# Kernel tuning notes

Measured on AMD Instinct MI355X. Metric: run time of the kernel, lower is better.

## Reference

```python
import math
import jax, jax.numpy as jnp
import numpy as np

EMBED_DIM = 512
NUM_HEADS = 8
HEAD_DIM = EMBED_DIM // NUM_HEADS
NUM_EDGE_TYPES = 10
N = 2048  # nodes
B = 1


def setup_inputs() -> dict:
    key = jax.random.key(0)
    ks = jax.random.split(key, 8)
    s = 1.0 / math.sqrt(EMBED_DIM)
    return {
        "query": jax.random.normal(ks[0], (N, B, EMBED_DIM), jnp.float32),
        "key": jax.random.normal(ks[1], (N, B, EMBED_DIM), jnp.float32),
        "value": jax.random.normal(ks[2], (N, B, EMBED_DIM), jnp.float32),
        "edge_id_mat": jax.random.randint(ks[3], (N, N), 0, NUM_EDGE_TYPES, jnp.int32),
        "in_proj_weight": jax.random.normal(ks[4], (3 * EMBED_DIM, EMBED_DIM), jnp.float32) * s,
        "in_proj_bias": jnp.zeros((3 * EMBED_DIM,), jnp.float32),
        "out_proj_weight": jax.random.normal(ks[5], (EMBED_DIM, EMBED_DIM), jnp.float32) * s,
        "out_proj_bias": jnp.zeros((EMBED_DIM,), jnp.float32),
        "edge_embs_K": jax.random.normal(ks[6], (NUM_EDGE_TYPES, HEAD_DIM), jnp.float32),
    }


def reference(query, key, value, edge_id_mat, in_proj_weight, in_proj_bias,
              out_proj_weight, out_proj_bias, edge_embs_K):
    L, Bsz, E = query.shape
    H, hd = NUM_HEADS, HEAD_DIM
    w_q, w_k, w_v = jnp.split(in_proj_weight, 3, axis=0)
    b_q, b_k, b_v = jnp.split(in_proj_bias, 3)
    q = query @ w_q.T + b_q   # (L, B, E)
    k = key @ w_k.T + b_k
    v = value @ w_v.T + b_v

    def split_heads(x):
        # (L, B, E) -> (B*H, L, hd)  (matches torch view(L, B*H, hd).transpose(0,1))
        return x.reshape(L, Bsz * H, hd).transpose(1, 0, 2)

    q = split_heads(q) / math.sqrt(hd)  # torch scales by sqrt(E=head_dim)
    k = split_heads(k)
    v = split_heads(v)

    attn = jnp.einsum('bnd,bmd->bnm', q, k)  # (B*H, L, L)

    # edge-type score bias: edge_attn[b,i,j] = q[b,i,:] . edge_embs_K[edge_id_mat[i,j], :]
    # computed efficiently as per-type scores then a gather (avoids (L,L,hd) tensor)
    type_scores = jnp.einsum('bnd,td->bnt', q, edge_embs_K)  # (B*H, L, T)
    idx = jnp.broadcast_to(edge_id_mat[None, :, :], attn.shape)
    edge_attn = jnp.take_along_axis(type_scores, idx, axis=2)  # (B*H, L, L)
    attn = jax.nn.softmax(attn + edge_attn, axis=-1)

    out = jnp.einsum('bnm,bmd->bnd', attn, v)           # (B*H, L, hd)
    out = out.transpose(1, 0, 2).reshape(L, Bsz, E)      # (L, B, E)
    out = out @ out_proj_weight.T + out_proj_bias
    return out
```

## Files before the change

### kernel.cpp

```cpp
#include <hip/hip_runtime.h>
#include <hip/hip_bf16.h>

#define NHEAD 8
#define SEQ   2048
#define HD    64
#define EMB   512
#define NTYPE 10
#define JSPLIT 4

#define QKV_NT (3 * EMB / 64)
#define QKV_MT (SEQ / 64)
#define QKV_BLOCKS (QKV_NT * QKV_MT)
#define PACK_BLOCKS (SEQ * SEQ / 4 / 256)

#define QSCALE 0.180336878f

typedef unsigned short u16;
typedef __attribute__((ext_vector_type(8))) short short8;
typedef __attribute__((ext_vector_type(4))) float float4v;

union F8 { short8 v; uint4 u4; u16 us[8]; };

__device__ __forceinline__ float bf2f(u16 u){
  union { unsigned u; float f; } w; w.u = ((unsigned)u) << 16; return w.f;
}
__device__ __forceinline__ u16 f2bf(float f){
  union { float f; unsigned u; } w; w.f = f;
  unsigned u = w.u;
  u += 0x7fffu + ((u >> 16) & 1u);
  return (u16)(u >> 16);
}
__device__ __forceinline__ unsigned cvtpk(float lo, float hi){
  union { __hip_bfloat162 b; unsigned u; } w;
  w.b = __float22bfloat162_rn(float2{lo, hi});
  return w.u;
}
__device__ __forceinline__ uint4 pk8(float4 a, float4 b){
  uint4 p; p.x = cvtpk(a.x, a.y); p.y = cvtpk(a.z, a.w);
           p.z = cvtpk(b.x, b.y); p.w = cvtpk(b.z, b.w);
  return p;
}

__global__ __launch_bounds__(256) void fused_prep_gemm(
    const float* __restrict__ q, const float* __restrict__ k, const float* __restrict__ v,
    const float* __restrict__ ipw, const float* __restrict__ ipb, const int* __restrict__ eid,
    u16* __restrict__ Qs, u16* __restrict__ Kb, u16* __restrict__ Vb,
    unsigned* __restrict__ eidp)
{
  const int b = blockIdx.x;
  const int t = threadIdx.x;

  if (b >= QKV_BLOCKS) {
    const int i = (b - QKV_BLOCKS) * 256 + t;
    int4 vv = ((const int4*)eid)[i];
    eidp[i] = (unsigned)(vv.x & 0xff) | ((unsigned)(vv.y & 0xff) << 8) |
              ((unsigned)(vv.z & 0xff) << 16) | ((unsigned)(vv.w & 0xff) << 24);
    return;
  }

  __shared__ u16 As[64][72];
  __shared__ u16 Bs[64][72];

  const int nt = b % QKV_NT, mt = b / QKV_NT;
  const int n0 = nt * 64, m0 = mt * 64;
  const int z = n0 >> 9;
  const float* A = (z == 0) ? q : (z == 1) ? k : v;
  const float scale = (z == 0) ? QSCALE : 1.0f;

  const int w = t >> 6, lane = t & 63, lr = lane & 15, lg = lane >> 4;
  const int wm = w >> 1, wn = w & 1;
  const int srow = t >> 2, kb16 = (t & 3) * 16;

  float4v acc[2][2];
#pragma unroll
  for (int mi = 0; mi < 2; mi++)
#pragma unroll
    for (int ni = 0; ni < 2; ni++) acc[mi][ni] = (float4v){0.f, 0.f, 0.f, 0.f};

  const float* pa = A   + (size_t)(m0 + srow) * EMB + kb16;
  const float* pw = ipw + (size_t)(n0 + srow) * EMB + kb16;

  float4 a[4], bb[4];
#pragma unroll
  for (int j = 0; j < 4; j++) { a[j] = *(const float4*)(pa + j * 4); bb[j] = *(const float4*)(pw + j * 4); }

  for (int k0 = 0; k0 < EMB; k0 += 64) {
    *(uint4*)&As[srow][kb16]     = pk8(a[0], a[1]);
    *(uint4*)&As[srow][kb16 + 8] = pk8(a[2], a[3]);
    *(uint4*)&Bs[srow][kb16]     = pk8(bb[0], bb[1]);
    *(uint4*)&Bs[srow][kb16 + 8] = pk8(bb[2], bb[3]);
    __syncthreads();
    if (k0 + 64 < EMB) {
#pragma unroll
      for (int j = 0; j < 4; j++) {
        a[j]  = *(const float4*)(pa + k0 + 64 + j * 4);
        bb[j] = *(const float4*)(pw + k0 + 64 + j * 4);
      }
    }
    F8 af[2][2], bf_[2][2];
#pragma unroll
    for (int kc = 0; kc < 2; kc++) {
#pragma unroll
      for (int mi = 0; mi < 2; mi++)
        af[mi][kc].u4 = *(const uint4*)&As[wm * 32 + mi * 16 + lr][kc * 32 + lg * 8];
#pragma unroll
      for (int ni = 0; ni < 2; ni++)
        bf_[ni][kc].u4 = *(const uint4*)&Bs[wn * 32 + ni * 16 + lr][kc * 32 + lg * 8];
    }
#pragma unroll
    for (int kc = 0; kc < 2; kc++)
#pragma unroll
      for (int mi = 0; mi < 2; mi++)
#pragma unroll
        for (int ni = 0; ni < 2; ni++)
          acc[mi][ni] = __builtin_amdgcn_mfma_f32_16x16x32_bf16(af[mi][kc].v, bf_[ni][kc].v, acc[mi][ni], 0, 0, 0);
    __syncthreads();
  }

  u16* O = (z == 0) ? Qs : ((z == 1) ? Kb : Vb);
#pragma unroll
  for (int mi = 0; mi < 2; mi++) {
#pragma unroll
    for (int ni = 0; ni < 2; ni++) {
      const int n = n0 + wn * 32 + ni * 16 + lr;
      const int e = n & 511, h = e >> 6, d = e & 63;
      const float bias = ipb[n];
      const int mb = m0 + wm * 32 + mi * 16 + lg * 4;
      if (z < 2) {
#pragma unroll
        for (int r = 0; r < 4; r++)
          O[((size_t)h * SEQ + mb + r) * HD + d] = f2bf((acc[mi][ni][r] + bias) * scale);
      } else {
        ushort4 pk;
        pk.x = f2bf(acc[mi][ni][0] + bias); pk.y = f2bf(acc[mi][ni][1] + bias);
        pk.z = f2bf(acc[mi][ni][2] + bias); pk.w = f2bf(acc[mi][ni][3] + bias);
        *(ushort4*)(O + ((size_t)(h * HD + d)) * SEQ + mb) = pk;
      }
    }
  }
}

__global__ __launch_bounds__(256) void attn_kernel(
    const u16* __restrict__ Qs, const u16* __restrict__ Kb, const u16* __restrict__ Vb,
    const unsigned* __restrict__ eid32, const float* __restrict__ EK,
    u16* __restrict__ Upart, float* __restrict__ mpart, float* __restrict__ lpart)
{
  __shared__ u16 Kt[64][72];
  __shared__ u16 Vt[64][72];
  __shared__ u16 Pl[4][16][72];
  __shared__ float tsl[64][13];
  __shared__ float ekl[NTYPE][64];

  const int t = threadIdx.x;
  const int wave = t >> 6, lane = t & 63, lr = lane & 15, lg = lane >> 4;
  const int i0 = blockIdx.x * 64;
  const int h  = blockIdx.y;
  const int z  = blockIdx.z;

  for (int i = t; i < NTYPE * 64; i += 256) ekl[i >> 6][i & 63] = EK[i];
  __syncthreads();

  {
    const int row = t >> 2, tt = t & 3;
    const u16* qr = Qs + ((size_t)h * SEQ + i0 + row) * HD;
    float a0 = 0.f, a1 = 0.f, a2 = 0.f;
    for (int d0 = 0; d0 < HD; d0 += 8) {
      uint4 qq = *(const uint4*)(qr + d0);
      const u16* qu = (const u16*)&qq;
#pragma unroll
      for (int e = 0; e < 8; e++) {
        float qf = bf2f(qu[e]);
        a0 += qf * ekl[tt][d0 + e];
        a1 += qf * ekl[tt + 4][d0 + e];
        a2 += qf * ekl[(tt < 2) ? (tt + 8) : 8][d0 + e];
      }
    }
    tsl[row][tt] = a0; tsl[row][tt + 4] = a1;
    if (tt < 2) tsl[row][tt + 8] = a2;
  }

  F8 qf[2];
#pragma unroll
  for (int kc = 0; kc < 2; kc++)
    qf[kc].u4 = *(const uint4*)(Qs + ((size_t)h * SEQ + i0 + wave * 16 + lr) * HD + kc * 32 + lg * 8);

  float4v ao[4];
#pragma unroll
  for (int d = 0; d < 4; d++) ao[d] = (float4v){0.f, 0.f, 0.f, 0.f};
  float m_i = -1e30f, l_i = 0.f;

  const int srow = t >> 2, sdc = (t & 3) * 16;
  const int jbase = z * (SEQ / JSPLIT);
  const int NT = (SEQ / JSPLIT) / 64;
  const unsigned* erow = eid32 + (size_t)(i0 + wave * 16 + lr) * (SEQ / 4);

  uint4 kp0, kp1, vp0, vp1;
  unsigned ed[4], edn[4];
  {
    const u16* kp = Kb + ((size_t)h * SEQ + jbase + srow) * HD + sdc;
    kp0 = *(const uint4*)kp; kp1 = *(const uint4*)(kp + 8);
    const u16* vp = Vb + ((size_t)(h * HD + srow)) * SEQ + jbase + sdc;
    vp0 = *(const uint4*)vp; vp1 = *(const uint4*)(vp + 8);
    *(uint4*)&Kt[srow][sdc] = kp0; *(uint4*)&Kt[srow][sdc + 8] = kp1;
    *(uint4*)&Vt[srow][sdc] = vp0; *(uint4*)&Vt[srow][sdc + 8] = vp1;
    const int ej = jbase >> 2;
#pragma unroll
    for (int c = 0; c < 4; c++) ed[c] = erow[ej + c * 4 + lg];
  }

  for (int jt = 0; jt < NT; jt++) {
    __syncthreads();

    if (jt + 1 < NT) {
      const int jn = jbase + (jt + 1) * 64;
      const u16* kp = Kb + ((size_t)h * SEQ + jn + srow) * HD + sdc;
      kp0 = *(const uint4*)kp; kp1 = *(const uint4*)(kp + 8);
      const u16* vp = Vb + ((size_t)(h * HD + srow)) * SEQ + jn + sdc;
      vp0 = *(const uint4*)vp; vp1 = *(const uint4*)(vp + 8);
      const int ejn = jn >> 2;
#pragma unroll
      for (int c = 0; c < 4; c++) edn[c] = erow[ejn + c * 4 + lg];
    }

    float4v sacc[4];
#pragma unroll
    for (int c = 0; c < 4; c++) sacc[c] = (float4v){0.f, 0.f, 0.f, 0.f};
#pragma unroll
    for (int kc = 0; kc < 2; kc++) {
#pragma unroll
      for (int c = 0; c < 4; c++) {
        F8 kf; kf.u4 = *(const uint4*)&Kt[c * 16 + lr][kc * 32 + lg * 8];
        sacc[c] = __builtin_amdgcn_mfma_f32_16x16x32_bf16(kf.v, qf[kc].v, sacc[c], 0, 0, 0);
      }
    }

    float rmax = -1e30f;
#pragma unroll
    for (int c = 0; c < 4; c++) {
      const unsigned e = ed[c];
#pragma unroll
      for (int r = 0; r < 4; r++) {
        const float s = sacc[c][r] + tsl[wave * 16 + lr][(e >> (r * 8)) & 0xffu];
        sacc[c][r] = s;
        rmax = fmaxf(rmax, s);
      }
    }
    rmax = fmaxf(rmax, __shfl_xor(rmax, 16));
    rmax = fmaxf(rmax, __shfl_xor(rmax, 32));
    const float mnew = fmaxf(m_i, rmax);
    const float fct = exp2f(m_i - mnew);
    float rsum = 0.f;
#pragma unroll
    for (int c = 0; c < 4; c++) {
#pragma unroll
      for (int r = 0; r < 4; r++) {
        const float p = exp2f(sacc[c][r] - mnew);
        sacc[c][r] = p;
        rsum += p;
      }
    }
    rsum += __shfl_xor(rsum, 16);
    rsum += __shfl_xor(rsum, 32);
    l_i = l_i * fct + rsum;
    m_i = mnew;

#pragma unroll
    for (int c = 0; c < 4; c++) {
      uint2 pw;
      pw.x = cvtpk(sacc[c][0], sacc[c][1]);
      pw.y = cvtpk(sacc[c][2], sacc[c][3]);
      *(uint2*)&Pl[wave][lr][c * 16 + lg * 4] = pw;
    }
#pragma unroll
    for (int db = 0; db < 4; db++) {
#pragma unroll
      for (int r = 0; r < 4; r++) ao[db][r] *= fct;
    }
#pragma unroll
    for (int kc = 0; kc < 2; kc++) {
      F8 pf; pf.u4 = *(const uint4*)&Pl[wave][lr][kc * 32 + lg * 8];
#pragma unroll
      for (int db = 0; db < 4; db++) {
        F8 vf; vf.u4 = *(const uint4*)&Vt[db * 16 + lr][kc * 32 + lg * 8];
        ao[db] = __builtin_amdgcn_mfma_f32_16x16x32_bf16(vf.v, pf.v, ao[db], 0, 0, 0);
      }
    }

    __syncthreads();
    if (jt + 1 < NT) {
      *(uint4*)&Kt[srow][sdc] = kp0; *(uint4*)&Kt[srow][sdc + 8] = kp1;
      *(uint4*)&Vt[srow][sdc] = vp0; *(uint4*)&Vt[srow][sdc + 8] = vp1;
#pragma unroll
      for (int c = 0; c < 4; c++) ed[c] = edn[c];
    }
  }

  {
    const size_t base = (((size_t)z * NHEAD + h) * SEQ + i0) * HD;
    const int n = wave * 16 + lr;
#pragma unroll
    for (int db = 0; db < 4; db++) {
      uint2 pw;
      pw.x = cvtpk(ao[db][0], ao[db][1]);
      pw.y = cvtpk(ao[db][2], ao[db][3]);
      *(uint2*)(Upart + base + (size_t)n * HD + db * 16 + lg * 4) = pw;
    }
    if (lg == 0) {
      mpart[((size_t)z * NHEAD + h) * SEQ + i0 + n] = m_i;
      lpart[((size_t)z * NHEAD + h) * SEQ + i0 + n] = l_i;
    }
  }
}

__global__ __launch_bounds__(256) void combine_outproj(
    const u16* __restrict__ Upart, const float* __restrict__ mpart,
    const float* __restrict__ lpart, const float* __restrict__ opw,
    const float* __restrict__ opb, float* __restrict__ out)
{
  __shared__ u16 As[64][72];
  __shared__ u16 Bs[64][72];
  __shared__ float cww[JSPLIT][NHEAD][64];

  const int t = threadIdx.x;
  const int n0 = blockIdx.x * 64;
  const int m0 = blockIdx.y * 64;

  for (int idx = t; idx < NHEAD * 64; idx += 256) {
    const int hh = idx >> 6, nl = idx & 63;
    const int gn = m0 + nl;
    float mz[JSPLIT], wz[JSPLIT];
    float M = -1e30f;
#pragma unroll
    for (int zz = 0; zz < JSPLIT; zz++) {
      mz[zz] = mpart[((size_t)zz * NHEAD + hh) * SEQ + gn];
      M = fmaxf(M, mz[zz]);
    }
    float Ls = 0.f;
#pragma unroll
    for (int zz = 0; zz < JSPLIT; zz++) {
      wz[zz] = exp2f(mz[zz] - M);
      Ls += wz[zz] * lpart[((size_t)zz * NHEAD + hh) * SEQ + gn];
    }
    const float inv = 1.0f / Ls;
#pragma unroll
    for (int zz = 0; zz < JSPLIT; zz++) cww[zz][hh][nl] = wz[zz] * inv;
  }
  __syncthreads();

  const int w = t >> 6, lane = t & 63, lr = lane & 15, lg = lane >> 4;
  const int wm = w >> 1, wn = w & 1;
  const int srow = t >> 2, kb16 = (t & 3) * 16;

  float4v acc[2][2];
#pragma unroll
  for (int mi = 0; mi < 2; mi++)
#pragma unroll
    for (int ni = 0; ni < 2; ni++) acc[mi][ni] = (float4v){0.f, 0.f, 0.f, 0.f};

  const float* pw = opw + (size_t)(n0 + srow) * EMB + kb16;

  int hcur = kb16 >> 6, dcur = kb16 & 63;
  uint4 ua[JSPLIT][2];
#pragma unroll
  for (int zz = 0; zz < JSPLIT; zz++) {
    const u16* pu = Upart + (((size_t)zz * NHEAD + hcur) * SEQ + m0 + srow) * HD + dcur;
    ua[zz][0] = *(const uint4*)pu; ua[zz][1] = *(const uint4*)(pu + 8);
  }
  float4 bb[4];
#pragma unroll
  for (int j = 0; j < 4; j++) bb[j] = *(const float4*)(pw + j * 4);

  for (int k0 = 0; k0 < EMB; k0 += 64) {
    {
      float cc[16];
#pragma unroll
      for (int j = 0; j < 16; j++) cc[j] = 0.f;
#pragma unroll
      for (int zz = 0; zz < JSPLIT; zz++) {
        const float wgt = cww[zz][hcur][srow];
        F8 q0, q1; q0.u4 = ua[zz][0]; q1.u4 = ua[zz][1];
#pragma unroll
        for (int j = 0; j < 8; j++) {
          cc[j]     += wgt * bf2f((u16)q0.us[j]);
          cc[j + 8] += wgt * bf2f((u16)q1.us[j]);
        }
      }
      float4 c0 = {cc[0], cc[1], cc[2], cc[3]},   c1 = {cc[4], cc[5], cc[6], cc[7]};
      float4 c2 = {cc[8], cc[9], cc[10], cc[11]}, c3 = {cc[12], cc[13], cc[14], cc[15]};
      *(uint4*)&As[srow][kb16]     = pk8(c0, c1);
      *(uint4*)&As[srow][kb16 + 8] = pk8(c2, c3);
      *(uint4*)&Bs[srow][kb16]     = pk8(bb[0], bb[1]);
      *(uint4*)&Bs[srow][kb16 + 8] = pk8(bb[2], bb[3]);
    }
    __syncthreads();
    if (k0 + 64 < EMB) {
      const int e = k0 + 64 + kb16;
      hcur = e >> 6; dcur = e & 63;
#pragma unroll
      for (int zz = 0; zz < JSPLIT; zz++) {
        const u16* pu = Upart + (((size_t)zz * NHEAD + hcur) * SEQ + m0 + srow) * HD + dcur;
        ua[zz][0] = *(const uint4*)pu; ua[zz][1] = *(const uint4*)(pu + 8);
      }
#pragma unroll
      for (int j = 0; j < 4; j++) bb[j] = *(const float4*)(pw + k0 + 64 + j * 4);
    }
    F8 af[2][2], bf_[2][2];
#pragma unroll
    for (int kc = 0; kc < 2; kc++) {
#pragma unroll
      for (int mi = 0; mi < 2; mi++)
        af[mi][kc].u4 = *(const uint4*)&As[wm * 32 + mi * 16 + lr][kc * 32 + lg * 8];
#pragma unroll
      for (int ni = 0; ni < 2; ni++)
        bf_[ni][kc].u4 = *(const uint4*)&Bs[wn * 32 + ni * 16 + lr][kc * 32 + lg * 8];
    }
#pragma unroll
    for (int kc = 0; kc < 2; kc++)
#pragma unroll
      for (int mi = 0; mi < 2; mi++)
#pragma unroll
        for (int ni = 0; ni < 2; ni++)
          acc[mi][ni] = __builtin_amdgcn_mfma_f32_16x16x32_bf16(af[mi][kc].v, bf_[ni][kc].v, acc[mi][ni], 0, 0, 0);
    __syncthreads();
  }

#pragma unroll
  for (int mi = 0; mi < 2; mi++) {
#pragma unroll
    for (int ni = 0; ni < 2; ni++) {
      const int n = n0 + wn * 32 + ni * 16 + lr;
      const float bias = opb[n];
      const int mb = m0 + wm * 32 + mi * 16 + lg * 4;
#pragma unroll
      for (int r = 0; r < 4; r++)
        out[(size_t)(mb + r) * EMB + n] = acc[mi][ni][r] + bias;
    }
  }
}

extern "C" void kernel_launch(void* const* d_in, const int* in_sizes, int n_in,
                              void* d_out, int out_size, void* d_ws, size_t ws_size,
                              hipStream_t stream)
{
  const float* query = (const float*)d_in[0];
  const float* key_  = (const float*)d_in[1];
  const float* value = (const float*)d_in[2];
  const int*   eid   = (const int*)d_in[3];
  const float* ipw   = (const float*)d_in[4];
  const float* ipb   = (const float*)d_in[5];
  const float* opw   = (const float*)d_in[6];
  const float* opb   = (const float*)d_in[7];
  const float* ek    = (const float*)d_in[8];
  float* out = (float*)d_out;

  char* ws = (char*)d_ws;
  u16* Qs = (u16*)ws;              ws += (size_t)NHEAD * SEQ * HD * 2;
  u16* Kb = (u16*)ws;              ws += (size_t)NHEAD * SEQ * HD * 2;
  u16* Vb = (u16*)ws;              ws += (size_t)NHEAD * SEQ * HD * 2;
  unsigned* eidp = (unsigned*)ws;  ws += (size_t)SEQ * SEQ;
  u16* Upart = (u16*)ws;           ws += (size_t)JSPLIT * NHEAD * SEQ * HD * 2;
  float* mpart = (float*)ws;       ws += (size_t)JSPLIT * NHEAD * SEQ * 4;
  float* lpart = (float*)ws;       ws += (size_t)JSPLIT * NHEAD * SEQ * 4;

  fused_prep_gemm<<<dim3(QKV_BLOCKS + PACK_BLOCKS), dim3(256), 0, stream>>>(
      query, key_, value, ipw, ipb, eid, Qs, Kb, Vb, eidp);
  attn_kernel<<<dim3(SEQ / 64, NHEAD, JSPLIT), dim3(256), 0, stream>>>(
      Qs, Kb, Vb, eidp, ek, Upart, mpart, lpart);
  combine_outproj<<<dim3(EMB / 64, SEQ / 64), dim3(256), 0, stream>>>(
      Upart, mpart, lpart, opw, opb, out);
}
```

Baseline: 158.9 us.

## Remap block indices for XCD-aware L2 locality and shrink out-proj tiles

Block indices in all three kernels are remapped so that blocks sharing the same K/V head/split or the same input rows land on the same XCD (b&7 chiplet interleave), which should improve L2 reuse on the multi-die GPU. The combine/out-projection kernel moves from 64x64 to 32x64 tiles. That doubles its block count for better CU occupancy, at the cost of more redundant weight loads. The QKV GEMM mapping now groups 4 M tiles per XCD. For the packing blocks, b&7 decoding applies only below QKV_BLOCKS, so those are unaffected.

```diff
diff --git a/kernel.cpp b/kernel.cpp
--- a/kernel.cpp
+++ b/kernel.cpp
@@ -61,7 +61,8 @@
   __shared__ u16 As[64][72];
   __shared__ u16 Bs[64][72];
 
-  const int nt = b % QKV_NT, mt = b / QKV_NT;
+  const int X = b & 7, jb = b >> 3;
+  const int mt = X * 4 + (jb & 3), nt = jb >> 2;
   const int n0 = nt * 64, m0 = mt * 64;
   const int z = n0 >> 9;
   const float* A = (z == 0) ? q : (z == 1) ? k : v;
@@ -153,9 +154,12 @@
 
   const int t = threadIdx.x;
   const int wave = t >> 6, lane = t & 63, lr = lane & 15, lg = lane >> 4;
-  const int i0 = blockIdx.x * 64;
-  const int h  = blockIdx.y;
-  const int z  = blockIdx.z;
+  const int bb_ = blockIdx.x;
+  const int X = bb_ & 7, jj = bb_ >> 3;
+  const int p = X * 4 + (jj >> 5);
+  const int i0 = (jj & 31) * 64;
+  const int h  = p >> 2;
+  const int z  = p & 3;
 
   for (int i = t; i < NTYPE * 64; i += 256) ekl[i >> 6][i & 63] = EK[i];
   __syncthreads();
@@ -254,9 +258,9 @@
     for (int c = 0; c < 4; c++) {
 #pragma unroll
       for (int r = 0; r < 4; r++) {
-        const float p = exp2f(sacc[c][r] - mnew);
-        sacc[c][r] = p;
-        rsum += p;
+        const float p_ = exp2f(sacc[c][r] - mnew);
+        sacc[c][r] = p_;
+        rsum += p_;
       }
     }
     rsum += __shfl_xor(rsum, 16);
@@ -317,16 +321,18 @@
     const float* __restrict__ lpart, const float* __restrict__ opw,
     const float* __restrict__ opb, float* __restrict__ out)
 {
-  __shared__ u16 As[64][72];
+  __shared__ u16 As[32][72];
   __shared__ u16 Bs[64][72];
-  __shared__ float cww[JSPLIT][NHEAD][64];
+  __shared__ float cww[JSPLIT][NHEAD][32];
 
   const int t = threadIdx.x;
-  const int n0 = blockIdx.x * 64;
-  const int m0 = blockIdx.y * 64;
-
-  for (int idx = t; idx < NHEAD * 64; idx += 256) {
-    const int hh = idx >> 6, nl = idx & 63;
+  const int b = blockIdx.x;
+  const int X = b & 7, jb = b >> 3;
+  const int mt = X * 8 + (jb >> 3), nt = jb & 7;
+  const int m0 = mt * 32, n0 = nt * 64;
+
+  {
+    const int hh = t >> 5, nl = t & 31;
     const int gn = m0 + nl;
     float mz[JSPLIT], wz[JSPLIT];
     float M = -1e30f;
@@ -348,93 +354,75 @@
   __syncthreads();
 
   const int w = t >> 6, lane = t & 63, lr = lane & 15, lg = lane >> 4;
-  const int wm = w >> 1, wn = w & 1;
-  const int srow = t >> 2, kb16 = (t & 3) * 16;
-
-  float4v acc[2][2];
-#pragma unroll
-  for (int mi = 0; mi < 2; mi++)
-#pragma unroll
-    for (int ni = 0; ni < 2; ni++) acc[mi][ni] = (float4v){0.f, 0.f, 0.f, 0.f};
-
-  const float* pw = opw + (size_t)(n0 + srow) * EMB + kb16;
-
-  int hcur = kb16 >> 6, dcur = kb16 & 63;
-  uint4 ua[JSPLIT][2];
-#pragma unroll
-  for (int zz = 0; zz < JSPLIT; zz++) {
-    const u16* pu = Upart + (((size_t)zz * NHEAD + hcur) * SEQ + m0 + srow) * HD + dcur;
-    ua[zz][0] = *(const uint4*)pu; ua[zz][1] = *(const uint4*)(pu + 8);
-  }
-  float4 bb[4];
-#pragma unroll
-  for (int j = 0; j < 4; j++) bb[j] = *(const float4*)(pw + j * 4);
+  const int arow = t >> 3, akb = (t & 7) * 8;
+  const int brow = t >> 2, bkb = (t & 3) * 16;
+
+  float4v acc[2];
+#pragma unroll
+  for (int mi = 0; mi < 2; mi++) acc[mi] = (float4v){0.f, 0.f, 0.f, 0.f};
+
+  const float* pw = opw + (size_t)(n0 + brow) * EMB + bkb;
+
+  int hcur = akb >> 6, dcur = akb & 63;
+  uint4 ua[JSPLIT];
+#pragma unroll
+  for (int zz = 0; zz < JSPLIT; zz++)
+    ua[zz] = *(const uint4*)(Upart + (((size_t)zz * NHEAD + hcur) * SEQ + m0 + arow) * HD + dcur);
+  float4 bbv[4];
+#pragma unroll
+  for (int j = 0; j < 4; j++) bbv[j] = *(const float4*)(pw + j * 4);
 
   for (int k0 = 0; k0 < EMB; k0 += 64) {
     {
-      float cc[16];
-#pragma unroll
-      for (int j = 0; j < 16; j++) cc[j] = 0.f;
+      float cc[8];
+#pragma unroll
+      for (int j = 0; j < 8; j++) cc[j] = 0.f;
 #pragma unroll
       for (int zz = 0; zz < JSPLIT; zz++) {
-        const float wgt = cww[zz][hcur][srow];
-        F8 q0, q1; q0.u4 = ua[zz][0]; q1.u4 = ua[zz][1];
-#pragma unroll
-        for (int j = 0; j < 8; j++) {
-          cc[j]     += wgt * bf2f((u16)q0.us[j]);
-          cc[j + 8] += wgt * bf2f((u16)q1.us[j]);
-        }
-      }
-      float4 c0 = {cc[0], cc[1], cc[2], cc[3]},   c1 = {cc[4], cc[5], cc[6], cc[7]};
-      float4 c2 = {cc[8], cc[9], cc[10], cc[11]}, c3 = {cc[12], cc[13], cc[14], cc[15]};
-      *(uint4*)&As[srow][kb16]     = pk8(c0, c1);
-      *(uint4*)&As[srow][kb16 + 8] = pk8(c2, c3);
-      *(uint4*)&Bs[srow][kb16]     = pk8(bb[0], bb[1]);
-      *(uint4*)&Bs[srow][kb16 + 8] = pk8(bb[2], bb[3]);
+        const float wgt = cww[zz][hcur][arow];
+        F8 q0; q0.u4 = ua[zz];
+#pragma unroll
+        for (int j = 0; j < 8; j++) cc[j] += wgt * bf2f((u16)q0.us[j]);
+      }
+      float4 c0 = {cc[0], cc[1], cc[2], cc[3]}, c1 = {cc[4], cc[5], cc[6], cc[7]};
+      *(uint4*)&As[arow][akb] = pk8(c0, c1);
+      *(uint4*)&Bs[brow][bkb]     = pk8(bbv[0], bbv[1]);
+      *(uint4*)&Bs[brow][bkb + 8] = pk8(bbv[2], bbv[3]);
     }
     __syncthreads();
     if (k0 + 64 < EMB) {
-      const int e = k0 + 64 + kb16;
+      const int e = k0 + 64 + akb;
       hcur = e >> 6; dcur = e & 63;
 #pragma unroll
-      for (int zz = 0; zz < JSPLIT; zz++) {
-        const u16* pu = Upart + (((size_t)zz * NHEAD + hcur) * SEQ + m0 + srow) * HD + dcur;
-        ua[zz][0] = *(const uint4*)pu; ua[zz][1] = *(const uint4*)(pu + 8);
-      }
-#pragma unroll
-      for (int j = 0; j < 4; j++) bb[j] = *(const float4*)(pw + k0 + 64 + j * 4);
-    }
-    F8 af[2][2], bf_[2][2];
+      for (int zz = 0; zz < JSPLIT; zz++)
+        ua[zz] = *(const uint4*)(Upart + (((size_t)zz * NHEAD + hcur) * SEQ + m0 + arow) * HD + dcur);
+#pragma unroll
+      for (int j = 0; j < 4; j++) bbv[j] = *(const float4*)(pw + k0 + 64 + j * 4);
+    }
+    F8 af[2][2], bf_[2];
 #pragma unroll
     for (int kc = 0; kc < 2; kc++) {
 #pragma unroll
       for (int mi = 0; mi < 2; mi++)
-        af[mi][kc].u4 = *(const uint4*)&As[wm * 32 + mi * 16 + lr][kc * 32 + lg * 8];
-#pragma unroll
-      for (int ni = 0; ni < 2; ni++)
-        bf_[ni][kc].u4 = *(const uint4*)&Bs[wn * 32 + ni * 16 + lr][kc * 32 + lg * 8];
+        af[mi][kc].u4 = *(const uint4*)&As[mi * 16 + lr][kc * 32 + lg * 8];
+      bf_[kc].u4 = *(const uint4*)&Bs[w * 16 + lr][kc * 32 + lg * 8];
     }
 #pragma unroll
     for (int kc = 0; kc < 2; kc++)
 #pragma unroll
       for (int mi = 0; mi < 2; mi++)
-#pragma unroll
-        for (int ni = 0; ni < 2; ni++)
-          acc[mi][ni] = __builtin_amdgcn_mfma_f32_16x16x32_bf16(af[mi][kc].v, bf_[ni][kc].v, acc[mi][ni], 0, 0, 0);
-    __syncthreads();
-  }
-
+        acc[mi] = __builtin_amdgcn_mfma_f32_16x16x32_bf16(af[mi][kc].v, bf_[kc].v, acc[mi], 0, 0, 0);
+    __syncthreads();
+  }
+
+  const int n = n0 + w * 16 + lr;
+  const float bias = opb[n];
 #pragma unroll
   for (int mi = 0; mi < 2; mi++) {
-#pragma unroll
-    for (int ni = 0; ni < 2; ni++) {
-      const int n = n0 + wn * 32 + ni * 16 + lr;
-      const float bias = opb[n];
-      const int mb = m0 + wm * 32 + mi * 16 + lg * 4;
-#pragma unroll
-      for (int r = 0; r < 4; r++)
-        out[(size_t)(mb + r) * EMB + n] = acc[mi][ni][r] + bias;
-    }
+    const int mb = m0 + mi * 16 + lg * 4;
+#pragma unroll
+    for (int r = 0; r < 4; r++)
+      out[(size_t)(mb + r) * EMB + n] = acc[mi][r] + bias;
   }
 }
 
@@ -464,8 +452,8 @@
 
   fused_prep_gemm<<<dim3(QKV_BLOCKS + PACK_BLOCKS), dim3(256), 0, stream>>>(
       query, key_, value, ipw, ipb, eid, Qs, Kb, Vb, eidp);
-  attn_kernel<<<dim3(SEQ / 64, NHEAD, JSPLIT), dim3(256), 0, stream>>>(
+  attn_kernel<<<dim3(SEQ / 64 * NHEAD * JSPLIT), dim3(256), 0, stream>>>(
       Qs, Kb, Vb, eidp, ek, Upart, mpart, lpart);
-  combine_outproj<<<dim3(EMB / 64, SEQ / 64), dim3(256), 0, stream>>>(
+  combine_outproj<<<dim3((SEQ / 32) * (EMB / 64)), dim3(256), 0, stream>>>(
       Upart, mpart, lpart, opw, opb, out);
 }
```

Result: faster. 150.0 us (-5.6%).
